# Optimization experiments

Measured on AMD Instinct MI355X. Metric: run time of the kernel, lower is better.

## Reference

```python
import jax, jax.numpy as jnp
import numpy as np

# Module constants (from init_kwargs)
MAP_BBOX = (-5.0, -5.0, 5.0, 5.0)  # h1, w1, h2, w2
V_BBOX = (0.0, 3.0)
MAP_RES = (64, 64)
V_RES = 8
XYZ_TO_H, XYZ_TO_W, XYZ_TO_V = 0, 1, 2
SCALE = 4
PCN_H = 64


def mish(x):
    return x * jnp.tanh(jax.nn.softplus(x))


def conv_d2(x, w):
    # 3x3 conv, dilation 2, padding 2, stride 1, no bias (NCHW / OIHW)
    return jax.lax.conv_general_dilated(
        x, w, window_strides=(1, 1), padding=((2, 2), (2, 2)),
        rhs_dilation=(2, 2), dimension_numbers=('NCHW', 'OIHW', 'NCHW'))


def maxpool3s2(x):
    # MaxPool2d(kernel=3, stride=2, padding=1); torch pads with -inf
    return jax.lax.reduce_window(
        x, -jnp.inf, jax.lax.max,
        window_dimensions=(1, 1, 3, 3), window_strides=(1, 1, 2, 2),
        padding=((0, 0), (0, 0), (1, 1), (1, 1)))


def setup_inputs() -> dict:
    key = jax.random.key(0)
    k1, k2, k3, k4, k5 = jax.random.split(key, 5)
    N, H, W = 64, 256, 256
    B = 8
    return {
        'rgb': jax.random.normal(k1, (N, 3, H, W), dtype=jnp.float32),
        'surf_xyz': jax.random.normal(k2, (N, 3, H, W), dtype=jnp.float32),
        'W1': jax.random.normal(k3, (PCN_H, 3, 3, 3), dtype=jnp.float32) * 0.1,
        'W2': jax.random.normal(k4, (PCN_H, PCN_H, 3, 3), dtype=jnp.float32) * 0.05,
        'index': jax.random.randint(k5, (N,), 0, B, dtype=jnp.int32),
        'batch_size': B,
    }


def reference(rgb, surf_xyz, W1, W2, index, batch_size):
    N, _, H, W = surf_xyz.shape
    s = SCALE
    Hs, Ws = H // s, W // s

    # avg_pool2d(rgb, 4)
    surf_rgb = rgb.reshape(N, 3, Hs, s, Ws, s).mean(axis=(3, 5))
    # subsampled xyz: surf_xyz[:, :, 2::4, 2::4]
    sxyz = surf_xyz[:, :, s // 2::s, s // 2::s]  # (N,3,Hs,Ws)
    _index = jnp.broadcast_to(index[:, None, None], (N, Hs, Ws))

    # rgb_conv_net: conv -> mish -> maxpool -> conv -> mish -> maxpool (dropout=0)
    feat = maxpool3s2(mish(conv_d2(rgb, W1)))
    feat = maxpool3s2(mish(conv_d2(feat, W2)))  # (N, h, Hs, Ws)

    # flatten  (valid_points is None path)
    hdim = feat.shape[1]
    flat_features = feat.transpose(0, 2, 3, 1).reshape(-1, hdim)   # (M, h)
    flat_xyz = sxyz.transpose(0, 2, 3, 1).reshape(-1, 3)           # (M, 3)
    flat_rgb = surf_rgb.transpose(0, 2, 3, 1).reshape(-1, 3)       # (M, 3)
    flat_index = _index.reshape(-1)                                # (M,)

    # coord_to_grid (float->int cast truncates toward zero, matching torch .long())
    map_h, map_w = MAP_RES
    h1, w1, h2, w2 = MAP_BBOX
    v1, v2 = V_BBOX
    hs = ((flat_xyz[:, XYZ_TO_H] - h1) * map_h / (h2 - h1)).astype(jnp.int32)
    ws = ((flat_xyz[:, XYZ_TO_W] - w1) * map_w / (w2 - w1)).astype(jnp.int32)
    vs = ((flat_xyz[:, XYZ_TO_V] - v1) * V_RES / (v2 - v1)).astype(jnp.int32)
    valid = ((hs >= 0) & (hs < map_h) & (ws >= 0) & (ws < map_w)
             & (vs >= 0) & (vs < V_RES))

    B, V = batch_size, V_RES
    P = B * V * map_h * map_w
    lin = ((flat_index * V + vs) * map_h + hs) * map_w + ws
    # route invalid points to a dummy segment that gets dropped
    lin_safe = jnp.where(valid, lin, P)

    sums = jax.ops.segment_sum(flat_features, lin_safe, num_segments=P + 1)[:P]
    rgbs = jax.ops.segment_sum(flat_rgb, lin_safe, num_segments=P + 1)[:P]
    counts = jax.ops.segment_sum(
        jnp.ones_like(lin_safe), lin_safe, num_segments=P + 1)[:P]

    feature_map = sums.reshape(B, V, map_h, map_w, hdim).transpose(0, 4, 1, 2, 3)
    rgb_map = rgbs.reshape(B, V, map_h, map_w, 3).transpose(0, 4, 1, 2, 3)
    feature_counts = counts.reshape(B, V, map_h, map_w)[:, None]
    return feature_map, feature_counts, rgb_map
```

## Files before the change

kernel.cpp:

```cpp
#include <hip/hip_runtime.h>
#include <hip/hip_bf16.h>
#include <math.h>

#define N_IMG 64
#define CH    64
#define F1_R  136
#define F1_C  136
#define F1_IMG_STRIDE ((size_t)F1_R * F1_C * 64)
#define F1_ROW_STRIDE (F1_C * 64)
#define FEAT1_BYTES ((size_t)N_IMG * F1_IMG_STRIDE * 2)
#define LINPT_BYTES (262144 * 4)
#define W2BF_BYTES (36864 * 2)

#define OUT_CNT_BASE 16777216
#define OUT_RGB_BASE 17039360

typedef short bf16x8 __attribute__((ext_vector_type(8)));
typedef float f32x4  __attribute__((ext_vector_type(4)));

__device__ __forceinline__ float fast_mish(float x) {
    float t = __expf(fminf(x, 30.0f));
    float n = t * (t + 2.0f);
    return x * (n / (n + 2.0f));
}

__device__ __forceinline__ unsigned short f2bf(float f) {
    unsigned u = __float_as_uint(f);
    unsigned r = (u + 0x7FFFu + ((u >> 16) & 1u)) >> 16;
    return (unsigned short)r;
}

__device__ __forceinline__ float bf2f(unsigned short h) {
    return __uint_as_float((unsigned)h << 16);
}

__global__ __launch_bounds__(256) void w2cvt_kernel(
    const float* __restrict__ w2, unsigned short* __restrict__ w2bf)
{
    int i = blockIdx.x * 256 + threadIdx.x;
    if (i < 36864) {
        int t  = i >> 12;
        int co = (i >> 6) & 63;
        int ci = i & 63;
        w2bf[i] = f2bf(w2[(co * 64 + ci) * 9 + t]);
    }
}

__global__ __launch_bounds__(256) void point_kernel(
    const float* __restrict__ rgb,
    const float* __restrict__ sxyz,
    const int*   __restrict__ index,
    float*       __restrict__ out,
    int*         __restrict__ lin_pt)
{
    int p = blockIdx.x * 256 + threadIdx.x;
    int n  = p >> 12;
    int r  = p & 4095;
    int hs = r >> 6;
    int ws = r & 63;

    int row = hs * 4 + 2, col = ws * 4 + 2;
    const float* sx = sxyz + (size_t)n * 3 * 65536;
    float X = sx[row * 256 + col];
    float Y = sx[65536 + row * 256 + col];
    float Z = sx[2 * 65536 + row * 256 + col];

    int hb = (int)(((X + 5.0f) * 64.0f) / 10.0f);
    int wb = (int)(((Y + 5.0f) * 64.0f) / 10.0f);
    int vb = (int)((Z * 8.0f) / 3.0f);
    bool valid = (hb >= 0) & (hb < 64) & (wb >= 0) & (wb < 64) & (vb >= 0) & (vb < 8);

    int b   = index[n];
    int lin = ((b * 8 + vb) * 64 + hb) * 64 + wb;
    lin_pt[p] = valid ? lin : -1;

    if (valid) {
        atomicAdd(out + OUT_CNT_BASE + lin, 1.0f);
        int rem = lin & 32767;
        #pragma unroll
        for (int c = 0; c < 3; c++) {
            const float* rg = rgb + (size_t)(n * 3 + c) * 65536;
            float s = 0.0f;
            #pragma unroll
            for (int i = 0; i < 4; i++)
                #pragma unroll
                for (int j = 0; j < 4; j++)
                    s += rg[(hs * 4 + i) * 256 + (ws * 4 + j)];
            atomicAdd(out + OUT_RGB_BASE + b * 98304 + c * 32768 + rem, s * 0.0625f);
        }
    }
}

__global__ __launch_bounds__(1024) void conv1_mfma_kernel(
    const float* __restrict__ rgb,
    const float* __restrict__ w1,
    __hip_bfloat16* __restrict__ feat1)
{
    int b2 = ((blockIdx.x & 7) << 9) + (blockIdx.x >> 3);
    const int n  = b2 >> 6;
    const int pr = b2 & 63;
    const int tid  = threadIdx.x;
    const int lane = tid & 63;
    const int w    = tid >> 6;

    __shared__ __align__(16) char smem[81920];
    unsigned short* wlds = (unsigned short*)smem;
    unsigned short* in_t = (unsigned short*)(smem + 4096);

    for (int i = tid; i < 2048; i += 1024) {
        int co = i >> 5, k = i & 31;
        wlds[i] = (k < 27) ? f2bf(w1[co * 27 + k]) : (unsigned short)0;
    }
    {
        const float* img = rgb + (size_t)n * 3 * 65536;
        for (int i = tid; i < 7144; i += 1024) {
            unsigned short v = 0;
            if (i < 7128) {
                int ci  = i / 2376;
                int rem = i - ci * 2376;
                int rr  = rem / 264;
                int cc  = rem - rr * 264;
                int gy  = 4 * pr - 3 + rr;
                int gx  = cc - 2;
                if (gy >= 0 && gy < 256 && gx >= 0 && gx < 256)
                    v = f2bf(img[ci * 65536 + gy * 256 + gx]);
            }
            in_t[i] = v;
        }
    }
    __syncthreads();

    int boff[8];
    #pragma unroll
    for (int j = 0; j < 8; j++) {
        int k = ((lane >> 4) << 3) + j;
        if (k < 27) {
            int ci = k / 9, t = k - 9 * ci, ky = t / 3, kx = t - 3 * ky;
            boff[j] = (ci * 2376 + 2 * ky * 264 + 2 * kx + (lane & 15)) * 2;
        } else {
            boff[j] = 7128 * 2;
        }
    }

    bf16x8 a[4];
    #pragma unroll
    for (int mt = 0; mt < 4; mt++)
        a[mt] = *reinterpret_cast<const bf16x8*>(
            wlds + (mt * 16 + (lane & 15)) * 32 + ((lane >> 4) << 3));

    f32x4 acc[5][4];
    #pragma unroll
    for (int tt = 0; tt < 5; tt++)
        #pragma unroll
        for (int mt = 0; mt < 4; mt++)
            acc[tt][mt] = (f32x4){0.f, 0.f, 0.f, 0.f};

    const char* in_b = (const char*)in_t;
    #pragma unroll
    for (int tt = 0; tt < 5; tt++) {
        int t5 = w * 5 + tt;
        int r  = t5 >> 4;
        int x0 = (t5 & 15) << 4;
        int base = (r * 264 + x0) * 2;
        unsigned short e[8];
        #pragma unroll
        for (int j = 0; j < 8; j++)
            e[j] = *reinterpret_cast<const unsigned short*>(in_b + base + boff[j]);
        bf16x8 b;
        #pragma unroll
        for (int j = 0; j < 8; j++) b[j] = (short)e[j];
        #pragma unroll
        for (int mt = 0; mt < 4; mt++)
            acc[tt][mt] = __builtin_amdgcn_mfma_f32_16x16x32_bf16(a[mt], b, acc[tt][mt], 0, 0, 0);
    }

    __syncthreads();

    unsigned short* pool = (unsigned short*)smem;
    const int ybase = 4 * pr - 1;

    const int r_pp  = tid >> 9;
    const int r_c   = (tid >> 2) & 127;
    const int r_cl0 = (tid & 3) * 8;

    #pragma unroll
    for (int p = 0; p < 2; p++) {
        #pragma unroll
        for (int tt = 0; tt < 5; tt++) {
            int t5 = w * 5 + tt;
            int r  = t5 >> 4;
            int x  = ((t5 & 15) << 4) + (lane & 15);
            bool dead = (ybase + r) < 0;
            #pragma unroll
            for (int m2 = 0; m2 < 2; m2++) {
                int mt  = p * 2 + m2;
                int col = m2 * 16 + ((lane >> 4) << 2);
                unsigned long long pk = 0;
                #pragma unroll
                for (int q = 0; q < 4; q++) {
                    float v = dead ? -INFINITY : fast_mish(acc[tt][mt][q]);
                    pk |= (unsigned long long)f2bf(v) << (16 * q);
                }
                int byte = (((r * 256 + x) * 32) + col) * 2;
                byte ^= (x & 7) << 4;
                *reinterpret_cast<unsigned long long*>((char*)pool + byte) = pk;
            }
        }
        __syncthreads();
        {
            float m[8];
            #pragma unroll
            for (int j = 0; j < 8; j++) m[j] = -INFINITY;
            #pragma unroll
            for (int dy = 0; dy < 3; dy++) {
                int lr = 2 * r_pp + dy;
                #pragma unroll
                for (int dx = 0; dx < 3; dx++) {
                    int x = 2 * r_c - 1 + dx;
                    if (x < 0) continue;
                    int byte = ((((lr * 256) + x) * 32) + r_cl0) * 2;
                    byte ^= (x & 7) << 4;
                    bf16x8 v = *reinterpret_cast<const bf16x8*>((char*)pool + byte);
                    #pragma unroll
                    for (int j = 0; j < 8; j++)
                        m[j] = fmaxf(m[j], bf2f((unsigned short)v[j]));
                }
            }
            bf16x8 vpk;
            #pragma unroll
            for (int j = 0; j < 8; j++) vpk[j] = (short)f2bf(m[j]);
            *reinterpret_cast<bf16x8*>((unsigned short*)(feat1
                + (size_t)n * F1_IMG_STRIDE
                + (size_t)(2 * pr + r_pp + 4) * F1_ROW_STRIDE
                + (size_t)(r_c + 4) * 64 + p * 32 + r_cl0)) = vpk;
        }
        __syncthreads();
    }
}

__global__ __launch_bounds__(512, 4) void conv2_mfma_kernel(
    const __hip_bfloat16* __restrict__ feat1,
    const unsigned short* __restrict__ w2bf,
    __hip_bfloat16* __restrict__ pre2,
    int n0)
{
    int b2 = ((blockIdx.x & 7) << 8) + (blockIdx.x >> 3);
    const int nl  = b2 >> 6;
    const int ch2 = (b2 >> 5) & 1;
    const int rq  = b2 & 31;
    const int n   = n0 + nl;
    const int tid  = threadIdx.x;
    const int lane = tid & 63;
    const int w    = tid >> 6;
    const int lrow = w >> 1;
    const int chalf = w & 1;
    const int y = 4 * rq + lrow;

    __shared__ __align__(16) char smem[36864];

    {
        const unsigned* src = (const unsigned*)w2bf;
        for (int i2 = tid; i2 < 9216; i2 += 512) {
            int t    = i2 >> 10;
            int rem  = i2 & 1023;
            int co32 = rem >> 5;
            int ci2  = rem & 31;
            int byte = (((((t << 5) + co32) << 6) + (ci2 << 1)) << 1) ^ ((co32 & 7) << 4);
            *reinterpret_cast<unsigned*>(smem + byte) =
                src[((t << 6) + ch2 * 32 + co32) * 32 + ci2];
        }
    }
    __syncthreads();

    f32x4 acc[2][4];
    #pragma unroll
    for (int mt = 0; mt < 2; mt++)
        #pragma unroll
        for (int nt = 0; nt < 4; nt++)
            acc[mt][nt] = (f32x4){0.f, 0.f, 0.f, 0.f};

    const __hip_bfloat16* bbase = feat1 + (size_t)n * F1_IMG_STRIDE
        + ((size_t)(y + 2) * F1_C + (lane & 15) + chalf * 64 + 2) * 64
        + ((lane >> 4) << 3);

    #pragma unroll
    for (int ky = 0; ky < 3; ky++) {
        #pragma unroll
        for (int kx = 0; kx < 3; kx++) {
            const int t = ky * 3 + kx;
            #pragma unroll
            for (int s = 0; s < 2; s++) {
                bf16x8 a[2];
                #pragma unroll
                for (int mt = 0; mt < 2; mt++) {
                    int co32 = mt * 16 + (lane & 15);
                    int abyte = (((((t << 5) + co32) << 6) + (s << 5) + ((lane >> 4) << 3)) << 1)
                                ^ ((co32 & 7) << 4);
                    a[mt] = *reinterpret_cast<const bf16x8*>(smem + abyte);
                }
                const __hip_bfloat16* bp = bbase + (ky * 2 * F1_C + kx * 2) * 64 + s * 32;
                #pragma unroll
                for (int nt = 0; nt < 4; nt++) {
                    bf16x8 b = *reinterpret_cast<const bf16x8*>(bp + nt * 1024);
                    #pragma unroll
                    for (int mt = 0; mt < 2; mt++)
                        acc[mt][nt] = __builtin_amdgcn_mfma_f32_16x16x32_bf16(
                            a[mt], b, acc[mt][nt], 0, 0, 0);
                }
            }
        }
    }

    #pragma unroll
    for (int nt = 0; nt < 4; nt++) {
        int col = chalf * 64 + nt * 16 + (lane & 15);
        #pragma unroll
        for (int mt = 0; mt < 2; mt++) {
            int co4 = ch2 * 32 + mt * 16 + ((lane >> 4) << 2);
            unsigned long long pk = 0;
            #pragma unroll
            for (int r4 = 0; r4 < 4; r4++)
                pk |= (unsigned long long)f2bf(fast_mish(acc[mt][nt][r4])) << (16 * r4);
            *reinterpret_cast<unsigned long long*>(
                pre2 + (((size_t)(nl * 128 + y) * 128 + col) * 64 + co4)) = pk;
        }
    }
}

__global__ __launch_bounds__(256) void pool2_scatter_kernel(
    const __hip_bfloat16* __restrict__ pre2,
    const int*   __restrict__ lin_pt,
    float*       __restrict__ out,
    int n0)
{
    int b2 = ((blockIdx.x & 7) << 8) + (blockIdx.x >> 3);
    const int nl = b2 >> 6;
    const int ph = b2 & 63;
    const int pw  = threadIdx.x >> 2;
    const int cog = threadIdx.x & 3;

    int lin = lin_pt[((n0 + nl) << 12) + (ph << 6) + pw];
    if (lin < 0) return;

    float m[16];
    #pragma unroll
    for (int k = 0; k < 16; k++) m[k] = -INFINITY;

    #pragma unroll
    for (int dy = 0; dy < 3; dy++) {
        int yy = 2 * ph - 1 + dy;
        if (yy < 0 || yy > 127) continue;
        #pragma unroll
        for (int dx = 0; dx < 3; dx++) {
            int xx = 2 * pw - 1 + dx;
            if (xx < 0 || xx > 127) continue;
            const unsigned short* p = (const unsigned short*)(pre2
                + ((size_t)(nl * 128 + yy) * 128 + xx) * 64 + cog * 16);
            #pragma unroll
            for (int h = 0; h < 2; h++) {
                bf16x8 v = *reinterpret_cast<const bf16x8*>(p + h * 8);
                #pragma unroll
                for (int j = 0; j < 8; j++)
                    m[h * 8 + j] = fmaxf(m[h * 8 + j], bf2f((unsigned short)v[j]));
            }
        }
    }

    float* base = out + (size_t)(lin >> 15) * 2097152 + (lin & 32767);
    #pragma unroll
    for (int k = 0; k < 16; k++)
        atomicAdd(base + (size_t)(cog * 16 + k) * 32768, m[k]);
}

extern "C" void kernel_launch(void* const* d_in, const int* in_sizes, int n_in,
                              void* d_out, int out_size, void* d_ws, size_t ws_size,
                              hipStream_t stream)
{
    const float* rgb   = (const float*)d_in[0];
    const float* sxyz  = (const float*)d_in[1];
    const float* w1    = (const float*)d_in[2];
    const float* w2    = (const float*)d_in[3];
    const int*   index = (const int*)d_in[4];
    float* out = (float*)d_out;

    __hip_bfloat16* feat1 = (__hip_bfloat16*)d_ws;
    int* lin_pt = (int*)((char*)d_ws + FEAT1_BYTES);
    unsigned short* w2bf = (unsigned short*)((char*)d_ws + FEAT1_BYTES + LINPT_BYTES);
    __hip_bfloat16* pre2 = (__hip_bfloat16*)((char*)d_ws + FEAT1_BYTES + LINPT_BYTES + W2BF_BYTES);

    hipMemsetAsync(d_out, 0, (size_t)out_size * 4, stream);
    hipMemsetAsync(d_ws, 0, FEAT1_BYTES, stream);

    w2cvt_kernel<<<144, 256, 0, stream>>>(w2, w2bf);
    point_kernel<<<1024, 256, 0, stream>>>(rgb, sxyz, index, out, lin_pt);
    conv1_mfma_kernel<<<4096, 1024, 0, stream>>>(rgb, w1, feat1);
    for (int c = 0; c < 2; c++) {
        conv2_mfma_kernel<<<2048, 512, 0, stream>>>(feat1, w2bf, pre2, c * 32);
        pool2_scatter_kernel<<<2048, 256, 0, stream>>>(pre2, lin_pt, out, c * 32);
    }
}
```

Measured before the change: 1.255 ms.

## Remap conv1 tiles so each wave owns a column strip and pools rows in registers

The conv1 kernel now gives each wave a fixed 16-column strip across all 5 input rows, instead of a flattened tile index. This lets the vertical 3-row max of the pool run in registers before anything is written to LDS. Only the vertically pooled rows are stored to shared memory, covering all 64 channels in one pass, so the LDS buffer shrinks and the two-pass loop with its extra barriers goes away. The horizontal max is then read from LDS and written to feat1. It trades a larger live register set (mish values for 5 rows per tile) for less LDS traffic and fewer synchronisations.

New measurement: 1.220 ms. -2.7%, faster.

```diff
diff --git a/kernel.cpp b/kernel.cpp
--- a/kernel.cpp
+++ b/kernel.cpp
@@ -103,7 +103,7 @@
     const int lane = tid & 63;
     const int w    = tid >> 6;
 
-    __shared__ __align__(16) char smem[81920];
+    __shared__ __align__(16) char smem[65536];
     unsigned short* wlds = (unsigned short*)smem;
     unsigned short* in_t = (unsigned short*)(smem + 4096);
 
@@ -150,18 +150,15 @@
 
     f32x4 acc[5][4];
     #pragma unroll
-    for (int tt = 0; tt < 5; tt++)
+    for (int r = 0; r < 5; r++)
         #pragma unroll
         for (int mt = 0; mt < 4; mt++)
-            acc[tt][mt] = (f32x4){0.f, 0.f, 0.f, 0.f};
+            acc[r][mt] = (f32x4){0.f, 0.f, 0.f, 0.f};
 
     const char* in_b = (const char*)in_t;
     #pragma unroll
-    for (int tt = 0; tt < 5; tt++) {
-        int t5 = w * 5 + tt;
-        int r  = t5 >> 4;
-        int x0 = (t5 & 15) << 4;
-        int base = (r * 264 + x0) * 2;
+    for (int r = 0; r < 5; r++) {
+        int base = (r * 264 + (w << 4)) * 2;
         unsigned short e[8];
         #pragma unroll
         for (int j = 0; j < 8; j++)
@@ -171,70 +168,66 @@
         for (int j = 0; j < 8; j++) b[j] = (short)e[j];
         #pragma unroll
         for (int mt = 0; mt < 4; mt++)
-            acc[tt][mt] = __builtin_amdgcn_mfma_f32_16x16x32_bf16(a[mt], b, acc[tt][mt], 0, 0, 0);
+            acc[r][mt] = __builtin_amdgcn_mfma_f32_16x16x32_bf16(a[mt], b, acc[r][mt], 0, 0, 0);
     }
 
     __syncthreads();
 
     unsigned short* pool = (unsigned short*)smem;
     const int ybase = 4 * pr - 1;
-
-    const int r_pp  = tid >> 9;
-    const int r_c   = (tid >> 2) & 127;
-    const int r_cl0 = (tid & 3) * 8;
-
-    #pragma unroll
-    for (int p = 0; p < 2; p++) {
-        #pragma unroll
-        for (int tt = 0; tt < 5; tt++) {
-            int t5 = w * 5 + tt;
-            int r  = t5 >> 4;
-            int x  = ((t5 & 15) << 4) + (lane & 15);
+    const int x = (w << 4) + (lane & 15);
+
+    #pragma unroll
+    for (int mt = 0; mt < 4; mt++) {
+        float mv[5][4];
+        #pragma unroll
+        for (int r = 0; r < 5; r++) {
             bool dead = (ybase + r) < 0;
             #pragma unroll
-            for (int m2 = 0; m2 < 2; m2++) {
-                int mt  = p * 2 + m2;
-                int col = m2 * 16 + ((lane >> 4) << 2);
-                unsigned long long pk = 0;
-                #pragma unroll
-                for (int q = 0; q < 4; q++) {
-                    float v = dead ? -INFINITY : fast_mish(acc[tt][mt][q]);
-                    pk |= (unsigned long long)f2bf(v) << (16 * q);
-                }
-                int byte = (((r * 256 + x) * 32) + col) * 2;
-                byte ^= (x & 7) << 4;
-                *reinterpret_cast<unsigned long long*>((char*)pool + byte) = pk;
+            for (int q = 0; q < 4; q++)
+                mv[r][q] = dead ? -INFINITY : fast_mish(acc[r][mt][q]);
+        }
+        #pragma unroll
+        for (int pp = 0; pp < 2; pp++) {
+            int co0 = mt * 16 + ((lane >> 4) << 2);
+            unsigned long long pk = 0;
+            #pragma unroll
+            for (int q = 0; q < 4; q++) {
+                float rm = fmaxf(fmaxf(mv[2 * pp][q], mv[2 * pp + 1][q]), mv[2 * pp + 2][q]);
+                pk |= (unsigned long long)f2bf(rm) << (16 * q);
             }
-        }
-        __syncthreads();
-        {
-            float m[8];
-            #pragma unroll
-            for (int j = 0; j < 8; j++) m[j] = -INFINITY;
-            #pragma unroll
-            for (int dy = 0; dy < 3; dy++) {
-                int lr = 2 * r_pp + dy;
-                #pragma unroll
-                for (int dx = 0; dx < 3; dx++) {
-                    int x = 2 * r_c - 1 + dx;
-                    if (x < 0) continue;
-                    int byte = ((((lr * 256) + x) * 32) + r_cl0) * 2;
-                    byte ^= (x & 7) << 4;
-                    bf16x8 v = *reinterpret_cast<const bf16x8*>((char*)pool + byte);
-                    #pragma unroll
-                    for (int j = 0; j < 8; j++)
-                        m[j] = fmaxf(m[j], bf2f((unsigned short)v[j]));
-                }
-            }
-            bf16x8 vpk;
-            #pragma unroll
-            for (int j = 0; j < 8; j++) vpk[j] = (short)f2bf(m[j]);
-            *reinterpret_cast<bf16x8*>((unsigned short*)(feat1
-                + (size_t)n * F1_IMG_STRIDE
-                + (size_t)(2 * pr + r_pp + 4) * F1_ROW_STRIDE
-                + (size_t)(r_c + 4) * 64 + p * 32 + r_cl0)) = vpk;
-        }
-        __syncthreads();
+            int byte = (((pp * 256 + x) * 64) + co0) * 2;
+            byte ^= (x & 7) << 4;
+            *reinterpret_cast<unsigned long long*>((char*)pool + byte) = pk;
+        }
+    }
+    __syncthreads();
+
+    #pragma unroll
+    for (int pp = 0; pp < 2; pp++) {
+        int c   = (tid >> 3) & 127;
+        int cl0 = (tid & 7) * 8;
+        float m[8];
+        #pragma unroll
+        for (int j = 0; j < 8; j++) m[j] = -INFINITY;
+        #pragma unroll
+        for (int dx = 0; dx < 3; dx++) {
+            int xx = 2 * c - 1 + dx;
+            if (xx < 0) continue;
+            int byte = ((((pp * 256) + xx) * 64) + cl0) * 2;
+            byte ^= (xx & 7) << 4;
+            bf16x8 v = *reinterpret_cast<const bf16x8*>((char*)pool + byte);
+            #pragma unroll
+            for (int j = 0; j < 8; j++)
+                m[j] = fmaxf(m[j], bf2f((unsigned short)v[j]));
+        }
+        bf16x8 vpk;
+        #pragma unroll
+        for (int j = 0; j < 8; j++) vpk[j] = (short)f2bf(m[j]);
+        *reinterpret_cast<bf16x8*>((unsigned short*)(feat1
+            + (size_t)n * F1_IMG_STRIDE
+            + (size_t)(2 * pr + pp + 4) * F1_ROW_STRIDE
+            + (size_t)(c + 4) * 64 + cl0)) = vpk;
     }
 }
 
```
